# Performance work log

Measured on AMD Instinct MI355X. Metric: run time of the kernel, lower is better.

## Reference

```python
import jax, jax.numpy as jnp
import numpy as np

PIXELS_PER_CELL = (8, 8)
CELLS_PER_BLOCK = (2, 2)
ORIENTATIONS = 9
GRAY_W = jnp.array([0.2125, 0.7154, 0.0721], dtype=jnp.float32)  # skimage rgb2gray
EPS = 1e-5  # skimage L2-Hys eps


def setup_inputs() -> dict:
    key = jax.random.key(0)
    x = jax.random.uniform(key, (64, 512, 512, 3), dtype=jnp.float32)
    return {"x": x}


def _hog(x):
    # rgb2gray
    gray = jnp.einsum("bhwc,c->bhw", x, GRAY_W)  # [B,H,W]
    B, H, W = gray.shape
    pr, pc = PIXELS_PER_CELL
    br, bc = CELLS_PER_BLOCK
    O = ORIENTATIONS

    # skimage _hog_channel_gradient: central differences, zero at borders
    g_row = jnp.zeros_like(gray).at[:, 1:-1, :].set(gray[:, 2:, :] - gray[:, :-2, :])
    g_col = jnp.zeros_like(gray).at[:, :, 1:-1].set(gray[:, :, 2:] - gray[:, :, :-2])

    mag = jnp.hypot(g_row, g_col)
    ori = jnp.rad2deg(jnp.arctan2(g_row, g_col)) % 180.0  # unsigned orientation

    ncr, ncc = H // pr, W // pc
    mag = mag[:, : ncr * pr, : ncc * pc]
    ori = ori[:, : ncr * pr, : ncc * pc]

    spacing = 180.0 / O
    cell_area = float(pr * pc)
    # per-orientation-bin cell histograms: hard binning (skimage cell_hog)
    hists = []
    for o in range(O):
        lo, hi = spacing * o, spacing * (o + 1)
        contrib = jnp.where((ori >= lo) & (ori < hi), mag, 0.0)
        # sum over each pr x pc cell, divide by cell area
        h = contrib.reshape(B, ncr, pr, ncc, pc).sum(axis=(2, 4)) / cell_area
        hists.append(h)
    hist = jnp.stack(hists, axis=-1)  # [B, ncr, ncc, O]

    # overlapping blocks of cells, stride 1 cell
    nbr, nbc = ncr - br + 1, ncc - bc + 1
    block = jnp.stack(
        [jnp.stack([hist[:, r : r + nbr, c : c + nbc, :] for c in range(bc)], axis=3)
         for r in range(br)], axis=3)  # [B, nbr, nbc, br, bc, O]

    # L2-Hys normalization (skimage default block_norm)
    norm = jnp.sqrt(jnp.sum(block * block, axis=(3, 4, 5), keepdims=True) + EPS ** 2)
    blk = jnp.minimum(block / norm, 0.2)
    norm2 = jnp.sqrt(jnp.sum(blk * blk, axis=(3, 4, 5), keepdims=True) + EPS ** 2)
    blk = blk / norm2

    return blk.reshape(B, -1).astype(jnp.float32)


def reference(x):
    return _hog(x)
```

## Files before the change

kernel.cpp:

```cpp
#include <hip/hip_runtime.h>
#include <math.h>

#define IMG_H 512
#define IMG_W 512
#define NCELL 64
#define NORI 9

__device__ __forceinline__ float fdlibm_atanf(float x) {
#pragma clang fp contract(off)
    const float atanhi[4] = {4.6364760399e-01f, 7.8539812565e-01f,
                             9.8279368877e-01f, 1.5707962513e+00f};
    const float atanlo[4] = {5.0121582440e-09f, 3.7748947079e-08f,
                             3.4473217170e-08f, 7.5497894159e-08f};
    const float aT[11] = {
        3.3333334327e-01f, -2.0000000298e-01f, 1.4285714924e-01f,
       -1.1111110449e-01f,  9.0908870101e-02f, -7.6918758452e-02f,
        6.6610731184e-02f, -5.8335702866e-02f,  4.9768779427e-02f,
       -3.6531571299e-02f,  1.6285819933e-02f};
    const float one = 1.0f;

    int hx = __float_as_int(x);
    int ix = hx & 0x7fffffff;
    int id;
    if (ix >= 0x4c800000) {
        if (hx > 0) return atanhi[3] + atanlo[3];
        else        return -atanhi[3] - atanlo[3];
    }
    if (ix < 0x3ee00000) {
        if (ix < 0x39800000) {
            return x;
        }
        id = -1;
    } else {
        x = fabsf(x);
        if (ix < 0x3f980000) {
            if (ix < 0x3f300000) { id = 0; x = (2.0f * x - one) / (2.0f + x); }
            else                 { id = 1; x = (x - one) / (x + one); }
        } else {
            if (ix < 0x401c0000) { id = 2; x = (x - 1.5f) / (one + 1.5f * x); }
            else                 { id = 3; x = -1.0f / x; }
        }
    }
    float z = x * x;
    float w = z * z;
    float s1 = z * (aT[0] + w * (aT[2] + w * (aT[4] + w * (aT[6] + w * (aT[8] + w * aT[10])))));
    float s2 = w * (aT[1] + w * (aT[3] + w * (aT[5] + w * (aT[7] + w * aT[9]))));
    if (id < 0) return x - x * (s1 + s2);
    z = atanhi[id] - ((x * (s1 + s2) - atanlo[id]) - x);
    return (hx < 0) ? -z : z;
}

__device__ __forceinline__ float fdlibm_atan2f(float y, float x) {
#pragma clang fp contract(off)
    const float tiny   = 1.0e-30f;
    const float pi_o_2 = 1.5707963705e+00f;
    const float pi     = 3.1415927410e+00f;
    const float pi_lo  = -8.7422776573e-08f;

    int hx = __float_as_int(x), ix = hx & 0x7fffffff;
    int hy = __float_as_int(y), iy = hy & 0x7fffffff;
    if (hx == 0x3f800000) return fdlibm_atanf(y);
    int m = ((hy >> 31) & 1) | ((hx >> 30) & 2);

    if (iy == 0) {
        switch (m) {
            case 0:
            case 1: return y;
            case 2: return  pi + tiny;
            case 3: return -pi - tiny;
        }
    }
    if (ix == 0) return (hy < 0) ? -pi_o_2 - tiny : pi_o_2 + tiny;

    int k = (iy - ix) >> 23;
    float z;
    if (k > 26) {
        z = pi_o_2 + 0.5f * pi_lo;
        m &= 1;
    } else if (k < -26 && hx < 0) {
        z = 0.0f;
    } else {
        z = fdlibm_atanf(fabsf(y / x));
    }
    switch (m) {
        case 0:  return z;
        case 1:  return -z;
        case 2:  return pi - (z - pi_lo);
        default: return (z - pi_lo) - pi;
    }
}

__global__ __launch_bounds__(256) void hog_hist_kernel(const float* __restrict__ x,
                                                       float* __restrict__ hist) {
#pragma clang fp contract(off)
    const int bid = blockIdx.x;
    const int b   = bid >> 6;
    const int cr  = bid & 63;
    const int t   = threadIdx.x;
    const int h0  = cr * 8;

    __shared__ __align__(16) float g[10][IMG_W];
    __shared__ float cellHist[NCELL * NORI];

    for (int i = t; i < NCELL * NORI; i += 256) cellHist[i] = 0.0f;

    const float GW0 = 0.2125f, GW1 = 0.7154f, GW2 = 0.0721f;
    for (int gi = t; gi < 10 * 128; gi += 256) {
        const int rr = gi >> 7;
        const int h  = h0 - 1 + rr;
        if (h < 0 || h >= IMG_H) continue;
        const int grp = gi & 127;
        const float4* p4 = (const float4*)x + (size_t)(b * IMG_H + h) * (IMG_W * 3 / 4)
                           + (size_t)grp * 3;
        float4 a = p4[0], c = p4[1], d = p4[2];
        const int wg = grp * 4;
        g[rr][wg + 0] = __builtin_fmaf(a.z, GW2, __builtin_fmaf(a.y, GW1, a.x * GW0));
        g[rr][wg + 1] = __builtin_fmaf(c.y, GW2, __builtin_fmaf(c.x, GW1, a.w * GW0));
        g[rr][wg + 2] = __builtin_fmaf(d.x, GW2, __builtin_fmaf(c.w, GW1, c.z * GW0));
        g[rr][wg + 3] = __builtin_fmaf(d.w, GW2, __builtin_fmaf(d.z, GW1, d.y * GW0));
    }
    __syncthreads();

    const float RAD2DEG = (float)(180.0 / 3.14159265358979311600e+00);
    for (int pass = 0; pass < 2; ++pass) {
        const int w    = t + pass * 256;
        const int cell = w >> 3;
        for (int r = 0; r < 8; ++r) {
            const int h = h0 + r;
            float gr = 0.0f, gc = 0.0f;
            if (h >= 1 && h <= IMG_H - 2) gr = g[r + 2][w] - g[r][w];
            if (w >= 1 && w <= IMG_W - 2) gc = g[r + 1][w + 1] - g[r + 1][w - 1];
            const double dr = (double)gr, dc = (double)gc;
            const float mag = (float)sqrt(dr * dr + dc * dc);
            const float th  = fdlibm_atan2f(gr, gc);
            float m = fmodf(th * RAD2DEG, 180.0f);
            if (m < 0.0f) m += 180.0f;
            int o = (int)(m * 0.05f);
            if (o < 9) {
                if (m < 20.0f * (float)o) --o;
                else if (m >= 20.0f * (float)(o + 1)) ++o;
            }
            if (o >= 0 && o <= 8 && mag != 0.0f)
                atomicAdd(&cellHist[cell * NORI + o], mag);
        }
    }
    __syncthreads();

    float* hout = hist + (size_t)(b * NCELL + cr) * (NCELL * NORI);
    for (int i = t; i < NCELL * NORI; i += 256) hout[i] = cellHist[i] * 0.015625f;
}

__global__ __launch_bounds__(256) void hog_norm_kernel(const float* __restrict__ hist,
                                                       float* __restrict__ out) {
#pragma clang fp contract(off)
    const int bid = blockIdx.x;
    const int b   = bid / 63;
    const int r   = bid % 63;
    const int t   = threadIdx.x;

    __shared__ __align__(16) float hrow[2 * NCELL * NORI];
    __shared__ __align__(16) float orow[63 * 36];

    const float4* src = (const float4*)(hist + (size_t)(b * NCELL + r) * (NCELL * NORI));
    float4* dst = (float4*)hrow;
    for (int i = t; i < 288; i += 256) dst[i] = src[i];
    __syncthreads();

    const int c = t >> 2;
    const int l = t & 3;
    if (c < 63) {
        const int bi = l >> 1, bj = l & 1;
        const float* v = &hrow[(bi * NCELL + (c + bj)) * NORI];
        float vv[9];
        float ss = 0.0f;
#pragma unroll
        for (int k = 0; k < 9; ++k) { vv[k] = v[k]; ss += vv[k] * vv[k]; }
        ss += __shfl_xor(ss, 1, 64);
        ss += __shfl_xor(ss, 2, 64);
        const float n1 = sqrtf(ss + 1e-10f);
        float ss2 = 0.0f;
#pragma unroll
        for (int k = 0; k < 9; ++k) { vv[k] = fminf(vv[k] / n1, 0.2f); ss2 += vv[k] * vv[k]; }
        ss2 += __shfl_xor(ss2, 1, 64);
        ss2 += __shfl_xor(ss2, 2, 64);
        const float n2 = sqrtf(ss2 + 1e-10f);
        float* od = &orow[c * 36 + l * 9];
#pragma unroll
        for (int k = 0; k < 9; ++k) od[k] = vv[k] / n2;
    }
    __syncthreads();

    float4* og = (float4*)(out + (size_t)bid * (63 * 36));
    const float4* os = (const float4*)orow;
    for (int i = t; i < 567; i += 256) og[i] = os[i];
}

extern "C" void kernel_launch(void* const* d_in, const int* in_sizes, int n_in,
                              void* d_out, int out_size, void* d_ws, size_t ws_size,
                              hipStream_t stream) {
    const float* x = (const float*)d_in[0];
    float* out     = (float*)d_out;
    float* hist    = (float*)d_ws;

    hog_hist_kernel<<<dim3(64 * 64), dim3(256), 0, stream>>>(x, hist);
    hog_norm_kernel<<<dim3(64 * 63), dim3(256), 0, stream>>>(hist, out);
}
```

Before: 365.6 us.

## Use fast polynomial atan2 binning with exact fdlibm fallback near bin edges

Replaces the per-pixel fdlibm atan2f plus fmod binning with a short minimax polynomial atan on the octant-reduced ratio, and computes the orientation bin directly from it. Only pixels whose angle falls very close to a bin boundary take a non-inlined exact fdlibm path, which keeps bin assignments matching the reference. The double-precision hypot becomes a single-precision fmaf and sqrtf. This removes the long branchy atan and FP64 work from the hot loop, at the cost of divergence on the rare fallback and small magnitude rounding differences.

```diff
diff --git a/kernel.cpp b/kernel.cpp
--- a/kernel.cpp
+++ b/kernel.cpp
@@ -6,7 +6,7 @@
 #define NCELL 64
 #define NORI 9
 
-__device__ __forceinline__ float fdlibm_atanf(float x) {
+__device__ __noinline__ float fdlibm_atanf(float x) {
 #pragma clang fp contract(off)
     const float atanhi[4] = {4.6364760399e-01f, 7.8539812565e-01f,
                              9.8279368877e-01f, 1.5707962513e+00f};
@@ -50,7 +50,7 @@
     return (hx < 0) ? -z : z;
 }
 
-__device__ __forceinline__ float fdlibm_atan2f(float y, float x) {
+__device__ __noinline__ int fdlibm_bin(float y, float x) {
 #pragma clang fp contract(off)
     const float tiny   = 1.0e-30f;
     const float pi_o_2 = 1.5707963705e+00f;
@@ -59,35 +59,48 @@
 
     int hx = __float_as_int(x), ix = hx & 0x7fffffff;
     int hy = __float_as_int(y), iy = hy & 0x7fffffff;
-    if (hx == 0x3f800000) return fdlibm_atanf(y);
-    int m = ((hy >> 31) & 1) | ((hx >> 30) & 2);
-
-    if (iy == 0) {
-        switch (m) {
-            case 0:
-            case 1: return y;
-            case 2: return  pi + tiny;
-            case 3: return -pi - tiny;
-        }
-    }
-    if (ix == 0) return (hy < 0) ? -pi_o_2 - tiny : pi_o_2 + tiny;
-
-    int k = (iy - ix) >> 23;
-    float z;
-    if (k > 26) {
-        z = pi_o_2 + 0.5f * pi_lo;
-        m &= 1;
-    } else if (k < -26 && hx < 0) {
-        z = 0.0f;
-    } else {
-        z = fdlibm_atanf(fabsf(y / x));
-    }
-    switch (m) {
-        case 0:  return z;
-        case 1:  return -z;
-        case 2:  return pi - (z - pi_lo);
-        default: return (z - pi_lo) - pi;
-    }
+    float th;
+    if (hx == 0x3f800000) { th = fdlibm_atanf(y); }
+    else {
+        int m = ((hy >> 31) & 1) | ((hx >> 30) & 2);
+        if (iy == 0) {
+            switch (m) {
+                case 0:
+                case 1: th = y; break;
+                case 2: th =  pi + tiny; break;
+                default: th = -pi - tiny; break;
+            }
+        } else if (ix == 0) {
+            th = (hy < 0) ? -pi_o_2 - tiny : pi_o_2 + tiny;
+        } else {
+            int k = (iy - ix) >> 23;
+            float z;
+            int mm = m;
+            if (k > 26) {
+                z = pi_o_2 + 0.5f * pi_lo;
+                mm &= 1;
+            } else if (k < -26 && hx < 0) {
+                z = 0.0f;
+            } else {
+                z = fdlibm_atanf(fabsf(y / x));
+            }
+            switch (mm) {
+                case 0:  th = z; break;
+                case 1:  th = -z; break;
+                case 2:  th = pi - (z - pi_lo); break;
+                default: th = (z - pi_lo) - pi; break;
+            }
+        }
+    }
+    const float RAD2DEG = (float)(180.0 / 3.14159265358979311600e+00);
+    float m = fmodf(th * RAD2DEG, 180.0f);
+    if (m < 0.0f) m += 180.0f;
+    int o = (int)(m * 0.05f);
+    if (o < 9) {
+        if (m < 20.0f * (float)o) --o;
+        else if (m >= 20.0f * (float)(o + 1)) ++o;
+    }
+    return o;
 }
 
 __global__ __launch_bounds__(256) void hog_hist_kernel(const float* __restrict__ x,
@@ -121,7 +134,9 @@
     }
     __syncthreads();
 
-    const float RAD2DEG = (float)(180.0 / 3.14159265358979311600e+00);
+    const float PIF   = 3.14159265358979323846f;
+    const float PIO2F = 1.57079632679489662f;
+    const float PIO4F = 0.78539816339744831f;
     for (int pass = 0; pass < 2; ++pass) {
         const int w    = t + pass * 256;
         const int cell = w >> 3;
@@ -130,18 +145,34 @@
             float gr = 0.0f, gc = 0.0f;
             if (h >= 1 && h <= IMG_H - 2) gr = g[r + 2][w] - g[r][w];
             if (w >= 1 && w <= IMG_W - 2) gc = g[r + 1][w + 1] - g[r + 1][w - 1];
-            const double dr = (double)gr, dc = (double)gc;
-            const float mag = (float)sqrt(dr * dr + dc * dc);
-            const float th  = fdlibm_atan2f(gr, gc);
-            float m = fmodf(th * RAD2DEG, 180.0f);
-            if (m < 0.0f) m += 180.0f;
-            int o = (int)(m * 0.05f);
-            if (o < 9) {
-                if (m < 20.0f * (float)o) --o;
-                else if (m >= 20.0f * (float)(o + 1)) ++o;
-            }
-            if (o >= 0 && o <= 8 && mag != 0.0f)
-                atomicAdd(&cellHist[cell * NORI + o], mag);
+            const float mag = sqrtf(__builtin_fmaf(gr, gr, gc * gc));
+            if (mag == 0.0f) continue;
+
+            const float ax = fabsf(gc), ay = fabsf(gr);
+            const float mx = fmaxf(ax, ay), mn = fminf(ax, ay);
+            const bool red = mn > 0.4142135624f * mx;
+            const float num = red ? (mn - mx) : mn;
+            const float den = red ? (mn + mx) : mx;
+            const float xx  = num / den;
+            const float z   = xx * xx;
+            float y = __builtin_fmaf(
+                        __builtin_fmaf(
+                          __builtin_fmaf(8.05374449538e-2f, z, -1.38776856032e-1f),
+                          z, 1.99777106478e-1f),
+                        z, -3.33329491539e-1f);
+            float r0 = __builtin_fmaf(y * z, xx, xx);
+            if (red)        r0 = PIO4F + r0;
+            if (ay > ax)    r0 = PIO2F - r0;
+            if (gc < 0.0f)  r0 = PIF - r0;
+            if (gr < 0.0f)  r0 = PIF - r0;
+            const float q    = (r0 * 57.295779513082323f) * 0.05f;
+            int o            = (int)q;
+            const float frac = q - (float)o;
+            if (frac < 1e-4f || frac > 0.9999f || o > 8) {
+                o = fdlibm_bin(gr, gc);
+                if (o < 0 || o > 8) continue;
+            }
+            atomicAdd(&cellHist[cell * NORI + o], mag);
         }
     }
     __syncthreads();
```

New measurement: 336.5 us. 8.0% less time.
